# Optimization experiments

Measured on AMD Instinct MI355X. Metric: run time of the kernel, lower is better.

Reference implementation:

```python
import jax, jax.numpy as jnp
import numpy as np

EMBED = 32
HEADS = 8
HEAD_DIM = EMBED // HEADS  # 4


def setup_inputs() -> dict:
    key = jax.random.key(0)
    ks = jax.random.split(key, 12)
    N, Q, K = 4, 2048, 2048
    inp = {
        "query": jax.random.normal(ks[0], (N, Q, EMBED), dtype=jnp.float32),
        "key": jax.random.normal(ks[1], (N, K, EMBED), dtype=jnp.float32),
        "value": jax.random.normal(ks[2], (N, K, EMBED), dtype=jnp.float32),
        "mask": jnp.ones((N, 1, Q, K), dtype=jnp.int32),
        # nn.Linear params: W stored as (in, out) here; math y = x @ W + b
        "Wq": jax.random.normal(ks[3], (EMBED, EMBED), dtype=jnp.float32) / np.sqrt(EMBED),
        "bq": jax.random.normal(ks[4], (EMBED,), dtype=jnp.float32) * 0.01,
        "Wk": jax.random.normal(ks[5], (EMBED, EMBED), dtype=jnp.float32) / np.sqrt(EMBED),
        "bk": jax.random.normal(ks[6], (EMBED,), dtype=jnp.float32) * 0.01,
        "Wv": jax.random.normal(ks[7], (EMBED, EMBED), dtype=jnp.float32) / np.sqrt(EMBED),
        "bv": jax.random.normal(ks[8], (EMBED,), dtype=jnp.float32) * 0.01,
        "Wo": jax.random.normal(ks[9], (EMBED, EMBED), dtype=jnp.float32) / np.sqrt(EMBED),
        "bo": jax.random.normal(ks[10], (EMBED,), dtype=jnp.float32) * 0.01,
    }
    return inp


def reference(query, key, value, mask, Wq, bq, Wk, bk, Wv, bv, Wo, bo):
    N, Qlen, _ = query.shape
    Klen = key.shape[1]
    # linear projections
    q = (query @ Wq + bq).reshape(N, Qlen, HEADS, HEAD_DIM)
    k = (key @ Wk + bk).reshape(N, Klen, HEADS, HEAD_DIM)
    v = (value @ Wv + bv).reshape(N, Klen, HEADS, HEAD_DIM)
    # energy: [N, H, Q, K]
    energy = jnp.einsum("nqhd,nkhd->nhqk", q, k)
    energy = jnp.where(mask == 0, jnp.float32(-1e20), energy)
    # NOTE: original scales by sqrt(embedSize), not sqrt(headDim)
    attn = jax.nn.softmax(energy / jnp.sqrt(jnp.float32(EMBED)), axis=3)
    out = jnp.einsum("nhqv,nvhd->nqhd", attn, v).reshape(N, Qlen, EMBED)
    return out @ Wo + bo
```

## Files before the change

kernel.cpp:

```cpp
#include <hip/hip_runtime.h>

#define NB 4
#define SEQ 2048
#define EMB 32
#define HEADS 8
#define HD 4

typedef float v2f __attribute__((ext_vector_type(2)));
typedef unsigned int uint;

__device__ __forceinline__ v2f splat2(float x) { v2f r; r.x = x; r.y = x; return r; }
__device__ __forceinline__ v2f pkfma(v2f a, v2f b, v2f c) {
  return __builtin_elementwise_fma(a, b, c);
}

__global__ __launch_bounds__(256) void pack_proj_kernel(
    const int* __restrict__ mask, uint* __restrict__ pmw,
    const float* __restrict__ key, const float* __restrict__ value,
    const float* __restrict__ Wk, const float* __restrict__ bk,
    const float* __restrict__ Wv, const float* __restrict__ bv,
    float* __restrict__ Kp, float* __restrict__ Vp) {
  const int packBlocks = NB * SEQ * SEQ / 4 / 256;
  if (blockIdx.x < packBlocks) {
    int g = blockIdx.x * 256 + threadIdx.x;
    const int4 v = ((const int4*)mask)[g];
    uint nib = (uint)(v.x != 0) | ((uint)(v.y != 0) << 1) |
               ((uint)(v.z != 0) << 2) | ((uint)(v.w != 0) << 3);
    int lane = threadIdx.x & 63;
    uint w = nib << (4 * (lane & 7));
    w |= __shfl_xor(w, 1);
    w |= __shfl_xor(w, 2);
    w |= __shfl_xor(w, 4);
    if ((lane & 7) == 0) pmw[g >> 3] = w;
  } else {
    const int half = NB * SEQ / 8;
    int blk2 = blockIdx.x - packBlocks;
    bool isV = blk2 >= half;
    const float* X = isV ? value : key;
    const float* W = isV ? Wv : Wk;
    const float* b = isV ? bv : bk;
    float* P = isV ? Vp : Kp;
    int blk = isV ? (blk2 - half) : blk2;

    __shared__ float sW[EMB][EMB];
    __shared__ float sb[EMB];
    __shared__ float sX[8][EMB];
    int t = threadIdx.x;
    for (int i = t; i < EMB * EMB; i += 256) sW[i >> 5][i & 31] = W[i];
    if (t < EMB) sb[t] = b[t];
    size_t row0 = (size_t)blk * 8;
    int r = t >> 5, c = t & 31;
    sX[r][c] = X[(row0 + r) * EMB + c];
    __syncthreads();
    float acc = sb[c];
#pragma unroll
    for (int d = 0; d < EMB; ++d) acc = fmaf(sX[r][d], sW[d][c], acc);
    P[(row0 + r) * EMB + c] = acc;
  }
}

__device__ __forceinline__ void load_tile(
    const float*& kptr, const float*& vptr,
    float4 (&KK)[4], float4 (&VV)[4]) {
  KK[0] = *(const float4*)(kptr);
  KK[1] = *(const float4*)(kptr + EMB);
  KK[2] = *(const float4*)(kptr + 2 * EMB);
  KK[3] = *(const float4*)(kptr + 3 * EMB);
  VV[0] = *(const float4*)(vptr);
  VV[1] = *(const float4*)(vptr + EMB);
  VV[2] = *(const float4*)(vptr + 2 * EMB);
  VV[3] = *(const float4*)(vptr + 3 * EMB);
  kptr += 32 * EMB; vptr += 32 * EMB;
}

__device__ __forceinline__ void compute_tile(
    const float4 (&KK)[4], const float4 (&VV)[4],
    const v2f (&q2)[4][4], v2f (&l2)[4], v2f (&ac2)[4][4]) {
#pragma unroll
  for (int p = 0; p < 4; ++p) {
    v2f pf[4];
#pragma unroll
    for (int j = 0; j < 4; ++j) {
      const float4 kk = KK[j];
      v2f s = pkfma(q2[p][0], splat2(kk.x),
              pkfma(q2[p][1], splat2(kk.y),
              pkfma(q2[p][2], splat2(kk.z), q2[p][3] * splat2(kk.w))));
      pf[j].x = __builtin_amdgcn_exp2f(s.x);
      pf[j].y = __builtin_amdgcn_exp2f(s.y);
    }
    l2[p] += (pf[0] + pf[1]) + (pf[2] + pf[3]);
#pragma unroll
    for (int j = 0; j < 4; ++j) {
      const float4 vv = VV[j];
      ac2[p][0] = pkfma(pf[j], splat2(vv.x), ac2[p][0]);
      ac2[p][1] = pkfma(pf[j], splat2(vv.y), ac2[p][1]);
      ac2[p][2] = pkfma(pf[j], splat2(vv.z), ac2[p][2]);
      ac2[p][3] = pkfma(pf[j], splat2(vv.w), ac2[p][3]);
    }
  }
}

__device__ __forceinline__ void compute_tile_masked(
    const float4 (&KK)[4], const float4 (&VV)[4],
    const uint (&MW)[8], int ks4,
    const v2f (&q2)[4][4], v2f (&l2)[4], v2f (&ac2)[4][4]) {
#pragma unroll
  for (int p = 0; p < 4; ++p) {
    v2f pf[4];
#pragma unroll
    for (int j = 0; j < 4; ++j) {
      const float4 kk = KK[j];
      v2f s = pkfma(q2[p][0], splat2(kk.x),
              pkfma(q2[p][1], splat2(kk.y),
              pkfma(q2[p][2], splat2(kk.z), q2[p][3] * splat2(kk.w))));
      pf[j].x = ((MW[2 * p + 0] >> (ks4 + j)) & 1u) ? __builtin_amdgcn_exp2f(s.x) : 0.0f;
      pf[j].y = ((MW[2 * p + 1] >> (ks4 + j)) & 1u) ? __builtin_amdgcn_exp2f(s.y) : 0.0f;
    }
    l2[p] += (pf[0] + pf[1]) + (pf[2] + pf[3]);
#pragma unroll
    for (int j = 0; j < 4; ++j) {
      const float4 vv = VV[j];
      ac2[p][0] = pkfma(pf[j], splat2(vv.x), ac2[p][0]);
      ac2[p][1] = pkfma(pf[j], splat2(vv.y), ac2[p][1]);
      ac2[p][2] = pkfma(pf[j], splat2(vv.z), ac2[p][2]);
      ac2[p][3] = pkfma(pf[j], splat2(vv.w), ac2[p][3]);
    }
  }
}

__global__ __launch_bounds__(256, 2) void attn_kernel(
    const float* __restrict__ query, const uint* __restrict__ pmw,
    const float* __restrict__ Kp, const float* __restrict__ Vp,
    const float* __restrict__ Wq, const float* __restrict__ bq,
    const float* __restrict__ Wo, const float* __restrict__ bo,
    float* __restrict__ out) {
  __shared__ float sWq[EMB][EMB];
  __shared__ float sWo[EMB][EMB];
  __shared__ float sbq[EMB];
  __shared__ float sbo[EMB];
  __shared__ float sX[16][EMB];
  __shared__ float sCtx[16][EMB + 1];
  __shared__ float sPart[2][16][EMB];
  __shared__ float sL[2][16][HEADS];

  int t = threadIdx.x;
  int n = blockIdx.x >> 7;
  int qt = blockIdx.x & 127;
  int qrow0 = qt * 16;

  int w = t >> 6;
  int octet = w >> 1;
  int kh = w & 1;
  int lane = t & 63;
  int h = lane & 7;
  int ks = lane >> 3;
  int ks4 = 4 * ks;
  int rbl = 8 * octet;

  for (int i = t; i < EMB * EMB; i += 256) {
    sWq[i >> 5][i & 31] = Wq[i];
    sWo[i >> 5][i & 31] = Wo[i];
  }
  if (t < EMB) { sbq[t] = bq[t]; sbo[t] = bo[t]; }
#pragma unroll
  for (int rr = 0; rr < 2; ++rr) {
    int r = (t >> 5) + 8 * rr, c = t & 31;
    sX[r][c] = query[((size_t)n * SEQ + qrow0 + r) * EMB + c];
  }
  __syncthreads();

  const float SC = 0.17677669529663687f * 1.4426950408889634f;
  v2f q2[4][4];
#pragma unroll
  for (int p = 0; p < 4; ++p)
#pragma unroll
    for (int d = 0; d < 4; ++d) q2[p][d] = splat2(sbq[4 * h + d]);
#pragma unroll
  for (int j = 0; j < EMB; ++j) {
    float w0 = sWq[j][4 * h + 0], w1 = sWq[j][4 * h + 1];
    float w2 = sWq[j][4 * h + 2], w3 = sWq[j][4 * h + 3];
#pragma unroll
    for (int p = 0; p < 4; ++p) {
      v2f x;
      x.x = sX[rbl + 2 * p + 0][j];
      x.y = sX[rbl + 2 * p + 1][j];
      q2[p][0] = pkfma(x, splat2(w0), q2[p][0]);
      q2[p][1] = pkfma(x, splat2(w1), q2[p][1]);
      q2[p][2] = pkfma(x, splat2(w2), q2[p][2]);
      q2[p][3] = pkfma(x, splat2(w3), q2[p][3]);
    }
  }
#pragma unroll
  for (int p = 0; p < 4; ++p)
#pragma unroll
    for (int d = 0; d < 4; ++d) q2[p][d] *= splat2(SC);

  const uint* mbase = pmw + ((size_t)n * SEQ + qrow0 + rbl) * (SEQ / 32) + kh * 32;
  int wl = lane & 7, rl = lane >> 3;
  const uint* mr = mbase + (size_t)rl * 64;
  uint myand = mr[wl] & mr[wl + 8] & mr[wl + 16] & mr[wl + 24];
  bool allones = __all(myand == 0xFFFFFFFFu);

  const float* kptr = Kp + (size_t)n * SEQ * EMB + (size_t)kh * 1024 * EMB
                         + (size_t)ks4 * EMB + 4 * h;
  const float* vptr = Vp + (size_t)n * SEQ * EMB + (size_t)kh * 1024 * EMB
                         + (size_t)ks4 * EMB + 4 * h;

  v2f l2[4], ac2[4][4];
#pragma unroll
  for (int p = 0; p < 4; ++p) {
    l2[p] = splat2(0.0f);
#pragma unroll
    for (int d = 0; d < 4; ++d) ac2[p][d] = splat2(0.0f);
  }

  if (allones) {
    float4 ka[4], va[4], kb[4], vb[4];
    load_tile(kptr, vptr, ka, va);
    for (int i = 0; i < 15; ++i) {
      load_tile(kptr, vptr, kb, vb);
      compute_tile(ka, va, q2, l2, ac2);
      load_tile(kptr, vptr, ka, va);
      compute_tile(kb, vb, q2, l2, ac2);
    }
    load_tile(kptr, vptr, kb, vb);
    compute_tile(ka, va, q2, l2, ac2);
    compute_tile(kb, vb, q2, l2, ac2);
  } else {
    for (int tile = 0; tile < 32; ++tile) {
      float4 ka[4], va[4];
      load_tile(kptr, vptr, ka, va);
      uint MW[8];
#pragma unroll
      for (int rr = 0; rr < 8; ++rr) MW[rr] = mbase[(size_t)rr * 64 + tile];
      compute_tile_masked(ka, va, MW, ks4, q2, l2, ac2);
    }
  }

#pragma unroll
  for (int d = 8; d <= 32; d <<= 1) {
#pragma unroll
    for (int p = 0; p < 4; ++p) {
      l2[p].x += __shfl_xor(l2[p].x, d);
      l2[p].y += __shfl_xor(l2[p].y, d);
#pragma unroll
      for (int e = 0; e < 4; ++e) {
        ac2[p][e].x += __shfl_xor(ac2[p][e].x, d);
        ac2[p][e].y += __shfl_xor(ac2[p][e].y, d);
      }
    }
  }

#pragma unroll
  for (int p = 0; p < 4; ++p) {
    int r0 = rbl + 2 * p;
    if (ks < 4) {
      float vA = (ks == 0) ? ac2[p][0].x : (ks == 1) ? ac2[p][1].x
               : (ks == 2) ? ac2[p][2].x : ac2[p][3].x;
      float vB = (ks == 0) ? ac2[p][0].y : (ks == 1) ? ac2[p][1].y
               : (ks == 2) ? ac2[p][2].y : ac2[p][3].y;
      sPart[kh][r0 + 0][4 * h + ks] = vA;
      sPart[kh][r0 + 1][4 * h + ks] = vB;
    } else if (ks == 4) {
      sL[kh][r0 + 0][h] = l2[p].x;
      sL[kh][r0 + 1][h] = l2[p].y;
    }
  }
  __syncthreads();

#pragma unroll
  for (int rr = 0; rr < 2; ++rr) {
    int r = (t >> 5) + 8 * rr, c = t & 31, hh = (t & 31) >> 2;
    float num = sPart[0][r][c] + sPart[1][r][c];
    float den = sL[0][r][hh] + sL[1][r][hh];
    sCtx[r][c] = num * __builtin_amdgcn_rcpf(den);
  }
  __syncthreads();

#pragma unroll
  for (int rr = 0; rr < 2; ++rr) {
    int r = (t >> 5) + 8 * rr, e = t & 31;
    float o = sbo[e];
#pragma unroll
    for (int j = 0; j < EMB; ++j) o = fmaf(sCtx[r][j], sWo[j][e], o);
    out[((size_t)n * SEQ + qrow0 + r) * EMB + e] = o;
  }
}

extern "C" void kernel_launch(void* const* d_in, const int* in_sizes, int n_in,
                              void* d_out, int out_size, void* d_ws, size_t ws_size,
                              hipStream_t stream) {
  const float* query = (const float*)d_in[0];
  const float* key   = (const float*)d_in[1];
  const float* value = (const float*)d_in[2];
  const int*   mask  = (const int*)d_in[3];
  const float* Wq = (const float*)d_in[4];
  const float* bq = (const float*)d_in[5];
  const float* Wk = (const float*)d_in[6];
  const float* bk = (const float*)d_in[7];
  const float* Wv = (const float*)d_in[8];
  const float* bv = (const float*)d_in[9];
  const float* Wo = (const float*)d_in[10];
  const float* bo = (const float*)d_in[11];
  float* out = (float*)d_out;

  float* Kp = (float*)d_ws;
  float* Vp = Kp + (size_t)NB * SEQ * EMB;
  uint* pmw = (uint*)(Vp + (size_t)NB * SEQ * EMB);

  const int packBlocks = NB * SEQ * SEQ / 4 / 256;
  const int projBlocks = 2 * NB * SEQ / 8;
  pack_proj_kernel<<<dim3(packBlocks + projBlocks), dim3(256), 0, stream>>>(
      mask, pmw, key, value, Wk, bk, Wv, bv, Kp, Vp);
  attn_kernel<<<dim3(NB * (SEQ / 16)), dim3(256), 0, stream>>>(
      query, pmw, Kp, Vp, Wq, bq, Wo, bo, out);
}
```

Measured before the change: 58.98 us.

## Split key range four ways per block, use inline packed-FP32 asm, reorder tile loop

Blocks grow from 256 to 512 threads, and each block splits the key sequence into four 512-key quarters instead of two halves, then reduces four partial sums in shared memory. The packed FMA, add and multiply operations are forced to v_pk_* instructions through inline asm. The tile compute loop is reordered so each key/value vector is splatted once and processed across all row pairs. The manual double-buffered K/V prefetch is dropped, which gives more waves for latency hiding but risks less instruction-level overlap and higher register pressure under launch_bounds(512,2).

```diff
diff --git a/kernel.cpp b/kernel.cpp
--- a/kernel.cpp
+++ b/kernel.cpp
@@ -10,8 +10,21 @@
 typedef unsigned int uint;
 
 __device__ __forceinline__ v2f splat2(float x) { v2f r; r.x = x; r.y = x; return r; }
+
 __device__ __forceinline__ v2f pkfma(v2f a, v2f b, v2f c) {
-  return __builtin_elementwise_fma(a, b, c);
+  v2f d;
+  asm("v_pk_fma_f32 %0, %1, %2, %3" : "=v"(d) : "v"(a), "v"(b), "v"(c));
+  return d;
+}
+__device__ __forceinline__ v2f pkadd(v2f a, v2f b) {
+  v2f d;
+  asm("v_pk_add_f32 %0, %1, %2" : "=v"(d) : "v"(a), "v"(b));
+  return d;
+}
+__device__ __forceinline__ v2f pkmul(v2f a, v2f b) {
+  v2f d;
+  asm("v_pk_mul_f32 %0, %1, %2" : "=v"(d) : "v"(a), "v"(b));
+  return d;
 }
 
 __global__ __launch_bounds__(256) void pack_proj_kernel(
@@ -77,25 +90,24 @@
     const float4 (&KK)[4], const float4 (&VV)[4],
     const v2f (&q2)[4][4], v2f (&l2)[4], v2f (&ac2)[4][4]) {
 #pragma unroll
-  for (int p = 0; p < 4; ++p) {
-    v2f pf[4];
-#pragma unroll
-    for (int j = 0; j < 4; ++j) {
-      const float4 kk = KK[j];
-      v2f s = pkfma(q2[p][0], splat2(kk.x),
-              pkfma(q2[p][1], splat2(kk.y),
-              pkfma(q2[p][2], splat2(kk.z), q2[p][3] * splat2(kk.w))));
-      pf[j].x = __builtin_amdgcn_exp2f(s.x);
-      pf[j].y = __builtin_amdgcn_exp2f(s.y);
-    }
-    l2[p] += (pf[0] + pf[1]) + (pf[2] + pf[3]);
-#pragma unroll
-    for (int j = 0; j < 4; ++j) {
-      const float4 vv = VV[j];
-      ac2[p][0] = pkfma(pf[j], splat2(vv.x), ac2[p][0]);
-      ac2[p][1] = pkfma(pf[j], splat2(vv.y), ac2[p][1]);
-      ac2[p][2] = pkfma(pf[j], splat2(vv.z), ac2[p][2]);
-      ac2[p][3] = pkfma(pf[j], splat2(vv.w), ac2[p][3]);
+  for (int j = 0; j < 4; ++j) {
+    const float4 kk = KK[j];
+    const float4 vv = VV[j];
+    v2f kx = splat2(kk.x), ky = splat2(kk.y), kz = splat2(kk.z), kw = splat2(kk.w);
+    v2f vx = splat2(vv.x), vy = splat2(vv.y), vz = splat2(vv.z), vw = splat2(vv.w);
+#pragma unroll
+    for (int p = 0; p < 4; ++p) {
+      v2f s = pkfma(q2[p][0], kx,
+              pkfma(q2[p][1], ky,
+              pkfma(q2[p][2], kz, pkmul(q2[p][3], kw))));
+      v2f pf;
+      pf.x = __builtin_amdgcn_exp2f(s.x);
+      pf.y = __builtin_amdgcn_exp2f(s.y);
+      l2[p] = pkadd(l2[p], pf);
+      ac2[p][0] = pkfma(pf, vx, ac2[p][0]);
+      ac2[p][1] = pkfma(pf, vy, ac2[p][1]);
+      ac2[p][2] = pkfma(pf, vz, ac2[p][2]);
+      ac2[p][3] = pkfma(pf, vw, ac2[p][3]);
     }
   }
 }
@@ -105,30 +117,29 @@
     const uint (&MW)[8], int ks4,
     const v2f (&q2)[4][4], v2f (&l2)[4], v2f (&ac2)[4][4]) {
 #pragma unroll
-  for (int p = 0; p < 4; ++p) {
-    v2f pf[4];
-#pragma unroll
-    for (int j = 0; j < 4; ++j) {
-      const float4 kk = KK[j];
-      v2f s = pkfma(q2[p][0], splat2(kk.x),
-              pkfma(q2[p][1], splat2(kk.y),
-              pkfma(q2[p][2], splat2(kk.z), q2[p][3] * splat2(kk.w))));
-      pf[j].x = ((MW[2 * p + 0] >> (ks4 + j)) & 1u) ? __builtin_amdgcn_exp2f(s.x) : 0.0f;
-      pf[j].y = ((MW[2 * p + 1] >> (ks4 + j)) & 1u) ? __builtin_amdgcn_exp2f(s.y) : 0.0f;
-    }
-    l2[p] += (pf[0] + pf[1]) + (pf[2] + pf[3]);
-#pragma unroll
-    for (int j = 0; j < 4; ++j) {
-      const float4 vv = VV[j];
-      ac2[p][0] = pkfma(pf[j], splat2(vv.x), ac2[p][0]);
-      ac2[p][1] = pkfma(pf[j], splat2(vv.y), ac2[p][1]);
-      ac2[p][2] = pkfma(pf[j], splat2(vv.z), ac2[p][2]);
-      ac2[p][3] = pkfma(pf[j], splat2(vv.w), ac2[p][3]);
-    }
-  }
-}
-
-__global__ __launch_bounds__(256, 2) void attn_kernel(
+  for (int j = 0; j < 4; ++j) {
+    const float4 kk = KK[j];
+    const float4 vv = VV[j];
+    v2f kx = splat2(kk.x), ky = splat2(kk.y), kz = splat2(kk.z), kw = splat2(kk.w);
+    v2f vx = splat2(vv.x), vy = splat2(vv.y), vz = splat2(vv.z), vw = splat2(vv.w);
+#pragma unroll
+    for (int p = 0; p < 4; ++p) {
+      v2f s = pkfma(q2[p][0], kx,
+              pkfma(q2[p][1], ky,
+              pkfma(q2[p][2], kz, pkmul(q2[p][3], kw))));
+      v2f pf;
+      pf.x = ((MW[2 * p + 0] >> (ks4 + j)) & 1u) ? __builtin_amdgcn_exp2f(s.x) : 0.0f;
+      pf.y = ((MW[2 * p + 1] >> (ks4 + j)) & 1u) ? __builtin_amdgcn_exp2f(s.y) : 0.0f;
+      l2[p] = pkadd(l2[p], pf);
+      ac2[p][0] = pkfma(pf, vx, ac2[p][0]);
+      ac2[p][1] = pkfma(pf, vy, ac2[p][1]);
+      ac2[p][2] = pkfma(pf, vz, ac2[p][2]);
+      ac2[p][3] = pkfma(pf, vw, ac2[p][3]);
+    }
+  }
+}
+
+__global__ __launch_bounds__(512, 2) void attn_kernel(
     const float* __restrict__ query, const uint* __restrict__ pmw,
     const float* __restrict__ Kp, const float* __restrict__ Vp,
     const float* __restrict__ Wq, const float* __restrict__ bq,
@@ -140,8 +151,8 @@
   __shared__ float sbo[EMB];
   __shared__ float sX[16][EMB];
   __shared__ float sCtx[16][EMB + 1];
-  __shared__ float sPart[2][16][EMB];
-  __shared__ float sL[2][16][HEADS];
+  __shared__ float sPart[4][16][EMB];
+  __shared__ float sL[4][16][HEADS];
 
   int t = threadIdx.x;
   int n = blockIdx.x >> 7;
@@ -149,22 +160,21 @@
   int qrow0 = qt * 16;
 
   int w = t >> 6;
-  int octet = w >> 1;
-  int kh = w & 1;
+  int oc = w >> 2;
+  int kq = w & 3;
   int lane = t & 63;
   int h = lane & 7;
   int ks = lane >> 3;
   int ks4 = 4 * ks;
-  int rbl = 8 * octet;
-
-  for (int i = t; i < EMB * EMB; i += 256) {
+  int rbl = 8 * oc;
+
+  for (int i = t; i < EMB * EMB; i += 512) {
     sWq[i >> 5][i & 31] = Wq[i];
     sWo[i >> 5][i & 31] = Wo[i];
   }
   if (t < EMB) { sbq[t] = bq[t]; sbo[t] = bo[t]; }
-#pragma unroll
-  for (int rr = 0; rr < 2; ++rr) {
-    int r = (t >> 5) + 8 * rr, c = t & 31;
+  {
+    int r = t >> 5, c = t & 31;
     sX[r][c] = query[((size_t)n * SEQ + qrow0 + r) * EMB + c];
   }
   __syncthreads();
@@ -177,33 +187,38 @@
     for (int d = 0; d < 4; ++d) q2[p][d] = splat2(sbq[4 * h + d]);
 #pragma unroll
   for (int j = 0; j < EMB; ++j) {
-    float w0 = sWq[j][4 * h + 0], w1 = sWq[j][4 * h + 1];
-    float w2 = sWq[j][4 * h + 2], w3 = sWq[j][4 * h + 3];
+    v2f w0 = splat2(sWq[j][4 * h + 0]);
+    v2f w1 = splat2(sWq[j][4 * h + 1]);
+    v2f w2 = splat2(sWq[j][4 * h + 2]);
+    v2f w3 = splat2(sWq[j][4 * h + 3]);
 #pragma unroll
     for (int p = 0; p < 4; ++p) {
       v2f x;
       x.x = sX[rbl + 2 * p + 0][j];
       x.y = sX[rbl + 2 * p + 1][j];
-      q2[p][0] = pkfma(x, splat2(w0), q2[p][0]);
-      q2[p][1] = pkfma(x, splat2(w1), q2[p][1]);
-      q2[p][2] = pkfma(x, splat2(w2), q2[p][2]);
-      q2[p][3] = pkfma(x, splat2(w3), q2[p][3]);
-    }
-  }
-#pragma unroll
-  for (int p = 0; p < 4; ++p)
-#pragma unroll
-    for (int d = 0; d < 4; ++d) q2[p][d] *= splat2(SC);
-
-  const uint* mbase = pmw + ((size_t)n * SEQ + qrow0 + rbl) * (SEQ / 32) + kh * 32;
+      q2[p][0] = pkfma(x, w0, q2[p][0]);
+      q2[p][1] = pkfma(x, w1, q2[p][1]);
+      q2[p][2] = pkfma(x, w2, q2[p][2]);
+      q2[p][3] = pkfma(x, w3, q2[p][3]);
+    }
+  }
+  {
+    v2f sc = splat2(SC);
+#pragma unroll
+    for (int p = 0; p < 4; ++p)
+#pragma unroll
+      for (int d = 0; d < 4; ++d) q2[p][d] = pkmul(q2[p][d], sc);
+  }
+
+  const uint* mbase = pmw + ((size_t)n * SEQ + qrow0 + rbl) * (SEQ / 32) + kq * 16;
   int wl = lane & 7, rl = lane >> 3;
   const uint* mr = mbase + (size_t)rl * 64;
-  uint myand = mr[wl] & mr[wl + 8] & mr[wl + 16] & mr[wl + 24];
+  uint myand = mr[wl] & mr[wl + 8];
   bool allones = __all(myand == 0xFFFFFFFFu);
 
-  const float* kptr = Kp + (size_t)n * SEQ * EMB + (size_t)kh * 1024 * EMB
+  const float* kptr = Kp + (size_t)n * SEQ * EMB + (size_t)kq * 512 * EMB
                          + (size_t)ks4 * EMB + 4 * h;
-  const float* vptr = Vp + (size_t)n * SEQ * EMB + (size_t)kh * 1024 * EMB
+  const float* vptr = Vp + (size_t)n * SEQ * EMB + (size_t)kq * 512 * EMB
                          + (size_t)ks4 * EMB + 4 * h;
 
   v2f l2[4], ac2[4][4];
@@ -215,19 +230,13 @@
   }
 
   if (allones) {
-    float4 ka[4], va[4], kb[4], vb[4];
-    load_tile(kptr, vptr, ka, va);
-    for (int i = 0; i < 15; ++i) {
-      load_tile(kptr, vptr, kb, vb);
+    for (int i = 0; i < 16; ++i) {
+      float4 ka[4], va[4];
+      load_tile(kptr, vptr, ka, va);
       compute_tile(ka, va, q2, l2, ac2);
-      load_tile(kptr, vptr, ka, va);
-      compute_tile(kb, vb, q2, l2, ac2);
-    }
-    load_tile(kptr, vptr, kb, vb);
-    compute_tile(ka, va, q2, l2, ac2);
-    compute_tile(kb, vb, q2, l2, ac2);
+    }
   } else {
-    for (int tile = 0; tile < 32; ++tile) {
+    for (int tile = 0; tile < 16; ++tile) {
       float4 ka[4], va[4];
       load_tile(kptr, vptr, ka, va);
       uint MW[8];
@@ -259,27 +268,26 @@
                : (ks == 2) ? ac2[p][2].x : ac2[p][3].x;
       float vB = (ks == 0) ? ac2[p][0].y : (ks == 1) ? ac2[p][1].y
                : (ks == 2) ? ac2[p][2].y : ac2[p][3].y;
-      sPart[kh][r0 + 0][4 * h + ks] = vA;
-      sPart[kh][r0 + 1][4 * h + ks] = vB;
+      sPart[kq][r0 + 0][4 * h + ks] = vA;
+      sPart[kq][r0 + 1][4 * h + ks] = vB;
     } else if (ks == 4) {
-      sL[kh][r0 + 0][h] = l2[p].x;
-      sL[kh][r0 + 1][h] = l2[p].y;
+      sL[kq][r0 + 0][h] = l2[p].x;
+      sL[kq][r0 + 1][h] = l2[p].y;
     }
   }
   __syncthreads();
 
-#pragma unroll
-  for (int rr = 0; rr < 2; ++rr) {
-    int r = (t >> 5) + 8 * rr, c = t & 31, hh = (t & 31) >> 2;
-    float num = sPart[0][r][c] + sPart[1][r][c];
-    float den = sL[0][r][hh] + sL[1][r][hh];
+  {
+    int r = t >> 5, c = t & 31, hh = (t & 31) >> 2;
+    float num = (sPart[0][r][c] + sPart[1][r][c]) +
+                (sPart[2][r][c] + sPart[3][r][c]);
+    float den = (sL[0][r][hh] + sL[1][r][hh]) + (sL[2][r][hh] + sL[3][r][hh]);
     sCtx[r][c] = num * __builtin_amdgcn_rcpf(den);
   }
   __syncthreads();
 
-#pragma unroll
-  for (int rr = 0; rr < 2; ++rr) {
-    int r = (t >> 5) + 8 * rr, e = t & 31;
+  {
+    int r = t >> 5, e = t & 31;
     float o = sbo[e];
 #pragma unroll
     for (int j = 0; j < EMB; ++j) o = fmaf(sCtx[r][j], sWo[j][e], o);
@@ -312,6 +320,6 @@
   const int projBlocks = 2 * NB * SEQ / 8;
   pack_proj_kernel<<<dim3(packBlocks + projBlocks), dim3(256), 0, stream>>>(
       mask, pmw, key, value, Wk, bk, Wv, bv, Kp, Vp);
-  attn_kernel<<<dim3(NB * (SEQ / 16)), dim3(256), 0, stream>>>(
+  attn_kernel<<<dim3(NB * (SEQ / 16)), dim3(512), 0, stream>>>(
       query, pmw, Kp, Vp, Wq, bq, Wo, bo, out);
 }
```

New measurement: 75.10 us. 1.27x slower.
